# Kernel optimization log

Hardware: AMD Instinct MI355X
Metric: run time of the kernel (lower is better)

The kernel has to match this reference:

```python
import jax, jax.numpy as jnp
import numpy as np

DILATIONS = [1, 2, 4, 8, 12, 24]
NUM_ITER = 10
W1 = 0.3
EPS = 1e-8
# 8-neighborhood offsets of the one-hot 3x3 kernel (center excluded)
OFFSETS = [(0, 0), (0, 1), (0, 2), (1, 0), (1, 2), (2, 0), (2, 1), (2, 2)]


def resize_bilinear_ac(x, oh, ow):
    """Bilinear resize with align_corners=True on the last two dims."""
    H, W = x.shape[-2], x.shape[-1]
    ys = jnp.linspace(0.0, H - 1.0, oh)
    xs = jnp.linspace(0.0, W - 1.0, ow)
    y0 = jnp.floor(ys).astype(jnp.int32)
    y1 = jnp.minimum(y0 + 1, H - 1)
    wy = (ys - y0).astype(x.dtype)
    x0 = jnp.floor(xs).astype(jnp.int32)
    x1 = jnp.minimum(x0 + 1, W - 1)
    wx = (xs - x0).astype(x.dtype)
    r = x[..., y0, :] * (1.0 - wy)[:, None] + x[..., y1, :] * wy[:, None]
    return r[..., x0] * (1.0 - wx) + r[..., x1] * wx


def dilated_neighbors(x, dilations):
    """Replicate-pad + gather 8 dilated neighbors per dilation.
    x: [b,c,h,w] -> [b,c,8*len(dilations),h,w] (matches one-hot conv2d emulation)."""
    b, c, h, w = x.shape
    outs = []
    for d in dilations:
        xp = jnp.pad(x, ((0, 0), (0, 0), (d, d), (d, d)), mode='edge')
        for ki, kj in OFFSETS:
            outs.append(xp[:, :, d * ki:d * ki + h, d * kj:d * kj + w])
    return jnp.stack(outs, axis=2)


def make_pos(dilations):
    base = jnp.ones(8, dtype=jnp.float32)
    base = base.at[jnp.array([0, 2, 5, 7])].set(np.sqrt(2.0).astype(np.float32))
    return jnp.concatenate([base * d for d in dilations])  # [8*D]


def setup_inputs() -> dict:
    key = jax.random.key(0)
    k1, k2 = jax.random.split(key)
    imgs = jax.random.normal(k1, (1, 3, 224, 224), dtype=jnp.float32)
    masks = jax.random.uniform(k2, (1, 21, 56, 56), dtype=jnp.float32)
    return {"imgs": imgs, "masks": masks}


def reference(imgs, masks):
    b, c, h, w = imgs.shape
    # upsample masks to image resolution
    masks = resize_bilinear_ac(masks, h, w)
    # low-res branch (scale_factor=0.3, floor like torch)
    h2, w2 = int(h * 0.3), int(w * 0.3)
    imgs2 = resize_bilinear_ac(imgs, h2, w2)

    n2 = dilated_neighbors(imgs2, DILATIONS)                     # [1,3,K,h2,w2]
    abs2 = jnp.abs(n2 - imgs2[:, :, None])
    std2 = jnp.std(n2, axis=2, keepdims=True, ddof=1)
    aff2 = (-(abs2 / (std2 + EPS)) ** 2).mean(axis=1, keepdims=True)  # [1,1,K,h2,w2]

    n1 = dilated_neighbors(imgs, DILATIONS)                      # [1,3,K,h,w]
    abs1 = jnp.abs(n1 - imgs[:, :, None])
    std1 = jnp.std(n1, axis=2, keepdims=True, ddof=1)
    aff = (-(abs1 / (std1 + EPS) / W1) ** 2).mean(axis=1, keepdims=True)  # [1,1,K,h,w]

    pos = make_pos(DILATIONS)                                    # [K]
    pos_std = jnp.std(pos, ddof=1)
    pos_aff = -((pos / (pos_std + EPS) / W1) ** 2)               # [K]

    # squeeze(0) -> bilinear upsample -> unsqueeze(0)
    aff2_up = resize_bilinear_ac(aff2[0], h, w)[None]            # [1,1,K,h,w]

    aff_total = (jax.nn.softmax(aff, axis=2)
                 + jax.nn.softmax(aff2_up, axis=2)
                 + jax.nn.softmax(pos_aff)[None, None, :, None, None])

    for _ in range(NUM_ITER):
        nm = dilated_neighbors(masks, DILATIONS)                 # [1,21,K,h,w]
        masks = (nm * aff_total).sum(axis=2)
    return masks
```

## Files before the change

kernel.cpp:

```cpp
#include <hip/hip_runtime.h>
#include <hip/hip_fp16.h>
#include <math.h>

namespace {
constexpr int IH = 224, IW = 224;
constexpr int H2 = 67, W2 = 67;
constexpr int MH = 56, MW = 56;
constexpr int CI = 3, CM = 21;
constexpr int ND = 6;
constexpr int K = 48;
constexpr int HW = IH * IW;
constexpr int HW2 = H2 * W2;
constexpr float EPS = 1e-8f;
__device__ __constant__ int DILS_C[ND] = {1, 2, 4, 8, 12, 24};
}

struct PosArr { float v[K]; };

__device__ __forceinline__ float wsum64(float v) {
    #pragma unroll
    for (int off = 1; off < 64; off <<= 1) v += __shfl_xor(v, off);
    return v;
}

__global__ void k_img_down(const float* __restrict__ img, float* __restrict__ img2) {
    int t = blockIdx.x * blockDim.x + threadIdx.x;
    if (t >= CI * HW2) return;
    int c = t / HW2, r = t % HW2;
    int y = r / W2, x = r % W2;
    float fy = (float)y * ((float)(IH - 1) / (float)(H2 - 1));
    float fx = (float)x * ((float)(IW - 1) / (float)(W2 - 1));
    int y0 = (int)floorf(fy); int y1 = min(y0 + 1, IH - 1); float wy = fy - (float)y0;
    int x0 = (int)floorf(fx); int x1 = min(x0 + 1, IW - 1); float wx = fx - (float)x0;
    const float* p = img + c * HW;
    float v00 = p[y0 * IW + x0], v01 = p[y0 * IW + x1];
    float v10 = p[y1 * IW + x0], v11 = p[y1 * IW + x1];
    float r0 = v00 * (1.f - wy) + v10 * wy;
    float r1 = v01 * (1.f - wy) + v11 * wy;
    img2[t] = r0 * (1.f - wx) + r1 * wx;
}

__global__ void k_aff2(const float* __restrict__ img2, float* __restrict__ aff2) {
    int gtid = blockIdx.x * blockDim.x + threadIdx.x;
    int wave = gtid >> 6;
    int lane = threadIdx.x & 63;
    if (wave >= HW2) return;
    int t = wave;
    int y = t / W2, x = t % W2;

    int k = (lane < K) ? lane : (K - 1);
    int di = k >> 3, o = k & 7;
    int d = DILS_C[di];
    int ym = max(y - d, 0), yp = min(y + d, H2 - 1);
    int xm = max(x - d, 0), xp = min(x + d, W2 - 1);
    int ki = (0x22211000u >> (o * 4)) & 3;
    int kj = (0x21020210u >> (o * 4)) & 3;
    int ry = ki == 0 ? ym : (ki == 1 ? y : yp);
    int rx = kj == 0 ? xm : (kj == 1 ? x : xp);
    int nidx = ry * W2 + rx;

    float av = 0.f;
    #pragma unroll
    for (int c = 0; c < CI; ++c) {
        const float* p = img2 + c * HW2;
        float center = p[y * W2 + x];
        float v = p[nidx];
        float vv = (lane < K) ? v : 0.f;
        float s = wsum64(vv);
        float s2 = wsum64(vv * vv);
        float mean = s * (1.f / (float)K);
        float ss = s2 - (float)K * mean * mean;
        float stdv = sqrtf(fmaxf(ss, 0.f) * (1.f / (float)(K - 1)));
        float inv = 1.f / (stdv + EPS);
        float tt = fabsf(v - center) * inv;
        av += tt * tt;
    }
    if (lane < K) aff2[(size_t)t * K + k] = av;
}

__global__ void k_aff_total(const float* __restrict__ img,
                            const float* __restrict__ aff2,
                            __half* __restrict__ afft, PosArr pos) {
    int gid = blockIdx.x * blockDim.x + threadIdx.x;
    int t = gid >> 4;
    int lane = threadIdx.x & 15;
    if (t >= HW) return;
    int y = t / IW, x = t % IW;

    int nidx[3];
    int kk[3];
    #pragma unroll
    for (int s = 0; s < 3; ++s) {
        int k = lane + 16 * s;
        kk[s] = k;
        int di = k >> 3, o = k & 7;
        int d = DILS_C[di];
        int ki = (0x22211000u >> (o * 4)) & 3;
        int kj = (0x21020210u >> (o * 4)) & 3;
        int ym = max(y - d, 0), yp = min(y + d, IH - 1);
        int xm = max(x - d, 0), xp = min(x + d, IW - 1);
        int ry = ki == 0 ? ym : (ki == 1 ? y : yp);
        int rx = kj == 0 ? xm : (kj == 1 ? x : xp);
        nidx[s] = ry * IW + rx;
    }

    float av0 = 0.f, av1 = 0.f, av2 = 0.f;
    #pragma unroll
    for (int c = 0; c < CI; ++c) {
        const float* p = img + c * HW;
        float center = p[y * IW + x];
        float n0 = p[nidx[0]], n1 = p[nidx[1]], n2 = p[nidx[2]];
        float s1 = n0 + n1 + n2;
        float s2 = n0 * n0 + n1 * n1 + n2 * n2;
        #pragma unroll
        for (int off = 1; off < 16; off <<= 1) {
            s1 += __shfl_xor(s1, off, 16);
            s2 += __shfl_xor(s2, off, 16);
        }
        float mean = s1 * (1.f / (float)K);
        float ss = s2 - (float)K * mean * mean;
        float inv = 1.f / (sqrtf(fmaxf(ss, 0.f) * (1.f / (float)(K - 1))) + EPS);
        float t0 = fabsf(n0 - center) * inv; av0 += t0 * t0;
        float t1 = fabsf(n1 - center) * inv; av1 += t1 * t1;
        float t2 = fabsf(n2 - center) * inv; av2 += t2 * t2;
    }
    const float sc = -(1.f / (float)CI) / (0.3f * 0.3f);
    av0 *= sc; av1 *= sc; av2 *= sc;
    float m1 = fmaxf(av0, fmaxf(av1, av2));
    #pragma unroll
    for (int off = 1; off < 16; off <<= 1) m1 = fmaxf(m1, __shfl_xor(m1, off, 16));
    float e0 = expf(av0 - m1), e1 = expf(av1 - m1), e2 = expf(av2 - m1);
    float es = e0 + e1 + e2;
    #pragma unroll
    for (int off = 1; off < 16; off <<= 1) es += __shfl_xor(es, off, 16);
    float r1 = 1.f / es;

    float fy = (float)y * ((float)(H2 - 1) / (float)(IH - 1));
    float fx = (float)x * ((float)(W2 - 1) / (float)(IW - 1));
    int y0 = (int)floorf(fy); int y1 = min(y0 + 1, H2 - 1); float wy = fy - (float)y0;
    int x0 = (int)floorf(fx); int x1 = min(x0 + 1, W2 - 1); float wx = fx - (float)x0;
    const float* q00 = aff2 + (size_t)(y0 * W2 + x0) * K;
    const float* q01 = aff2 + (size_t)(y0 * W2 + x1) * K;
    const float* q10 = aff2 + (size_t)(y1 * W2 + x0) * K;
    const float* q11 = aff2 + (size_t)(y1 * W2 + x1) * K;
    float w00 = (1.f - wy) * (1.f - wx), w01 = (1.f - wy) * wx;
    float w10 = wy * (1.f - wx), w11 = wy * wx;
    const float sc2 = -(1.f / (float)CI);
    float b0 = (q00[kk[0]] * w00 + q01[kk[0]] * w01 + q10[kk[0]] * w10 + q11[kk[0]] * w11) * sc2;
    float b1 = (q00[kk[1]] * w00 + q01[kk[1]] * w01 + q10[kk[1]] * w10 + q11[kk[1]] * w11) * sc2;
    float b2 = (q00[kk[2]] * w00 + q01[kk[2]] * w01 + q10[kk[2]] * w10 + q11[kk[2]] * w11) * sc2;
    float m2 = fmaxf(b0, fmaxf(b1, b2));
    #pragma unroll
    for (int off = 1; off < 16; off <<= 1) m2 = fmaxf(m2, __shfl_xor(m2, off, 16));
    float f0 = expf(b0 - m2), f1 = expf(b1 - m2), f2 = expf(b2 - m2);
    float fs = f0 + f1 + f2;
    #pragma unroll
    for (int off = 1; off < 16; off <<= 1) fs += __shfl_xor(fs, off, 16);
    float r2 = 1.f / fs;

    __half* o = afft + (size_t)t * K;
    o[kk[0]] = __float2half(e0 * r1 + f0 * r2 + pos.v[kk[0]]);
    o[kk[1]] = __float2half(e1 * r1 + f1 * r2 + pos.v[kk[1]]);
    o[kk[2]] = __float2half(e2 * r1 + f2 * r2 + pos.v[kk[2]]);
}

__global__ void k_mask_up(const float* __restrict__ m, float* __restrict__ mu) {
    int t = blockIdx.x * blockDim.x + threadIdx.x;
    if (t >= CM * HW) return;
    int c = t / HW, r = t % HW;
    int y = r / IW, x = r % IW;
    float fy = (float)y * ((float)(MH - 1) / (float)(IH - 1));
    float fx = (float)x * ((float)(MW - 1) / (float)(IW - 1));
    int y0 = (int)floorf(fy); int y1 = min(y0 + 1, MH - 1); float wy = fy - (float)y0;
    int x0 = (int)floorf(fx); int x1 = min(x0 + 1, MW - 1); float wx = fx - (float)x0;
    const float* p = m + c * MH * MW;
    float v00 = p[y0 * MW + x0], v01 = p[y0 * MW + x1];
    float v10 = p[y1 * MW + x0], v11 = p[y1 * MW + x1];
    float r0 = v00 * (1.f - wy) + v10 * wy;
    float r1 = v01 * (1.f - wy) + v11 * wy;
    mu[t] = r0 * (1.f - wx) + r1 * wx;
}

__global__ __launch_bounds__(256) void k_prop(const float* __restrict__ min_,
                                              const __half* __restrict__ afft,
                                              float* __restrict__ mout) {
    __shared__ float L[13 * 224];
    int tid = threadIdx.x;
    int bid = blockIdx.x;
    int sw = (bid & 7) * 588 + (bid >> 3);
    int y = sw / 21;
    int c = sw - y * 21;

    int x = min(tid, IW - 1);
    int t = y * IW + x;
    uint4 w[6];
    {
        const uint4* aw = (const uint4*)(afft + (size_t)t * K);
        #pragma unroll
        for (int i = 0; i < 6; ++i) w[i] = aw[i];
    }

    const int ROW_DY[13] = {-24, -12, -8, -4, -2, -1, 0, 1, 2, 4, 8, 12, 24};
    const float* mc = min_ + (size_t)c * HW;
    for (int i = tid; i < 13 * 56; i += 256) {
        int r = i / 56;
        int xq = i - r * 56;
        int gy = min(max(y + ROW_DY[r], 0), IH - 1);
        *(float4*)(L + r * 224 + xq * 4) = ((const float4*)(mc + gy * IW))[xq];
    }
    __syncthreads();

    if (tid >= IW) return;

    const int DILS[ND] = {1, 2, 4, 8, 12, 24};
    const int RMI[ND] = {5, 4, 3, 2, 1, 0};
    const int RPI[ND] = {7, 8, 9, 10, 11, 12};
    const float* Lc = L + 6 * 224;

    float acc = 0.f;
    #pragma unroll
    for (int di = 0; di < ND; ++di) {
        int d = DILS[di];
        int cm = max(x - d, 0);
        int cp = min(x + d, IW - 1);
        const float* Lm = L + RMI[di] * 224;
        const float* Lp = L + RPI[di] * 224;
        const __half2* hp = (const __half2*)&w[di];
        float2 f01 = __half22float2(hp[0]);
        float2 f23 = __half22float2(hp[1]);
        float2 f45 = __half22float2(hp[2]);
        float2 f67 = __half22float2(hp[3]);
        acc += Lm[cm] * f01.x;
        acc += Lm[x]  * f01.y;
        acc += Lm[cp] * f23.x;
        acc += Lc[cm] * f23.y;
        acc += Lc[cp] * f45.x;
        acc += Lp[cm] * f45.y;
        acc += Lp[x]  * f67.x;
        acc += Lp[cp] * f67.y;
    }
    mout[(size_t)c * HW + t] = acc;
}

extern "C" void kernel_launch(void* const* d_in, const int* in_sizes, int n_in,
                              void* d_out, int out_size, void* d_ws, size_t ws_size,
                              hipStream_t stream) {
    const float* imgs  = (const float*)d_in[0];
    const float* masks = (const float*)d_in[1];
    float* out = (float*)d_out;

    float* ws = (float*)d_ws;
    float* imgs2 = ws;
    float* aff2  = imgs2 + 16384;
    __half* afft = (__half*)(aff2 + K * HW2);
    float* mA    = aff2 + K * HW2 + (K * HW) / 2;
    float* mB    = mA + (size_t)CM * HW;

    PosArr pos;
    {
        double pv[K];
        const int dil[ND] = {1, 2, 4, 8, 12, 24};
        const double s2 = sqrt(2.0);
        for (int di = 0; di < ND; ++di)
            for (int o = 0; o < 8; ++o) {
                double base = (o == 0 || o == 2 || o == 5 || o == 7) ? s2 : 1.0;
                pv[di * 8 + o] = base * (double)dil[di];
            }
        double sum = 0.0; for (int k = 0; k < K; ++k) sum += pv[k];
        double mean = sum / K;
        double ssd = 0.0; for (int k = 0; k < K; ++k) { double d0 = pv[k] - mean; ssd += d0 * d0; }
        double stdv = sqrt(ssd / (K - 1));
        double pa[K];
        double mx = -1e300;
        for (int k = 0; k < K; ++k) {
            double u = pv[k] / (stdv + 1e-8) / 0.3;
            pa[k] = -u * u;
            if (pa[k] > mx) mx = pa[k];
        }
        double es = 0.0, ev[K];
        for (int k = 0; k < K; ++k) { ev[k] = exp(pa[k] - mx); es += ev[k]; }
        for (int k = 0; k < K; ++k) pos.v[k] = (float)(ev[k] / es);
    }

    dim3 blk(256);
    k_img_down<<<(CI * HW2 + 255) / 256, blk, 0, stream>>>(imgs, imgs2);
    k_aff2<<<(HW2 * 64 + 255) / 256, blk, 0, stream>>>(imgs2, aff2);
    k_aff_total<<<(HW * 16 + 255) / 256, blk, 0, stream>>>(imgs, aff2, afft, pos);
    k_mask_up<<<(CM * HW + 255) / 256, blk, 0, stream>>>(masks, mA);

    float* bufs[2] = {mA, mB};
    const float* cur = mA;
    for (int i = 0; i < 10; ++i) {
        float* o = (i == 9) ? out : bufs[(i + 1) & 1];
        k_prop<<<4704, dim3(256), 0, stream>>>(cur, afft, o);
        cur = o;
    }
}
```

Baseline: 205.4 us.

## Process three row-channel tiles per block with register-prefetched next tile

Each propagation block now handles three (row, channel) work items instead of one. While computing the current item, it prefetches the next item's 13 mask rows into registers, then stores them to shared memory between two barriers. The grid shrinks threefold and launch bounds request higher occupancy. This aims to hide global load latency behind compute and amortise block launch cost. In exchange it adds register pressure and extra barriers, and leaves fewer blocks to spread across the GPU.

```diff
diff --git a/kernel.cpp b/kernel.cpp
--- a/kernel.cpp
+++ b/kernel.cpp
@@ -181,65 +181,109 @@
     mu[t] = r0 * (1.f - wx) + r1 * wx;
 }
 
-__global__ __launch_bounds__(256) void k_prop(const float* __restrict__ min_,
-                                              const __half* __restrict__ afft,
-                                              float* __restrict__ mout) {
+__global__ __launch_bounds__(256, 8) void k_prop(const float* __restrict__ min_,
+                                                 const __half* __restrict__ afft,
+                                                 float* __restrict__ mout) {
     __shared__ float L[13 * 224];
-    int tid = threadIdx.x;
-    int bid = blockIdx.x;
-    int sw = (bid & 7) * 588 + (bid >> 3);
-    int y = sw / 21;
-    int c = sw - y * 21;
-
-    int x = min(tid, IW - 1);
-    int t = y * IW + x;
-    uint4 w[6];
+    const int tid = threadIdx.x;
+    const int b = blockIdx.x;
+    const int base = (b & 7) * 588 + (b >> 3);
+    const int ROW_DY[13] = {-24, -12, -8, -4, -2, -1, 0, 1, 2, 4, 8, 12, 24};
+
     {
-        const uint4* aw = (const uint4*)(afft + (size_t)t * K);
-        #pragma unroll
-        for (int i = 0; i < 6; ++i) w[i] = aw[i];
-    }
-
-    const int ROW_DY[13] = {-24, -12, -8, -4, -2, -1, 0, 1, 2, 4, 8, 12, 24};
-    const float* mc = min_ + (size_t)c * HW;
-    for (int i = tid; i < 13 * 56; i += 256) {
-        int r = i / 56;
-        int xq = i - r * 56;
-        int gy = min(max(y + ROW_DY[r], 0), IH - 1);
-        *(float4*)(L + r * 224 + xq * 4) = ((const float4*)(mc + gy * IW))[xq];
+        int sw = base;
+        int y = sw / 21, c = sw - y * 21;
+        const float* mc = min_ + (size_t)c * HW;
+        for (int i = tid; i < 13 * 56; i += 256) {
+            int r = i / 56, q = i - r * 56;
+            int gy = min(max(y + ROW_DY[r], 0), IH - 1);
+            *(float4*)(L + r * 224 + q * 4) = ((const float4*)(mc + gy * IW))[q];
+        }
     }
     __syncthreads();
 
-    if (tid >= IW) return;
-
-    const int DILS[ND] = {1, 2, 4, 8, 12, 24};
-    const int RMI[ND] = {5, 4, 3, 2, 1, 0};
-    const int RPI[ND] = {7, 8, 9, 10, 11, 12};
-    const float* Lc = L + 6 * 224;
-
-    float acc = 0.f;
-    #pragma unroll
-    for (int di = 0; di < ND; ++di) {
-        int d = DILS[di];
-        int cm = max(x - d, 0);
-        int cp = min(x + d, IW - 1);
-        const float* Lm = L + RMI[di] * 224;
-        const float* Lp = L + RPI[di] * 224;
-        const __half2* hp = (const __half2*)&w[di];
-        float2 f01 = __half22float2(hp[0]);
-        float2 f23 = __half22float2(hp[1]);
-        float2 f45 = __half22float2(hp[2]);
-        float2 f67 = __half22float2(hp[3]);
-        acc += Lm[cm] * f01.x;
-        acc += Lm[x]  * f01.y;
-        acc += Lm[cp] * f23.x;
-        acc += Lc[cm] * f23.y;
-        acc += Lc[cp] * f45.x;
-        acc += Lp[cm] * f45.y;
-        acc += Lp[x]  * f67.x;
-        acc += Lp[cp] * f67.y;
-    }
-    mout[(size_t)c * HW + t] = acc;
+    #pragma unroll
+    for (int j = 0; j < 3; ++j) {
+        const int sw = base + j * 196;
+        const int y = sw / 21, c = sw - y * 21;
+
+        float4 s0, s1, s2;
+        if (j < 2) {
+            int sw2 = base + (j + 1) * 196;
+            int y2 = sw2 / 21, c2 = sw2 - y2 * 21;
+            const float* mc2 = min_ + (size_t)c2 * HW;
+            {
+                int i = tid; int r = i / 56, q = i - r * 56;
+                int gy = min(max(y2 + ROW_DY[r], 0), IH - 1);
+                s0 = ((const float4*)(mc2 + gy * IW))[q];
+            }
+            {
+                int i = tid + 256; int r = i / 56, q = i - r * 56;
+                int gy = min(max(y2 + ROW_DY[r], 0), IH - 1);
+                s1 = ((const float4*)(mc2 + gy * IW))[q];
+            }
+            if (tid < 216) {
+                int i = tid + 512; int r = i / 56, q = i - r * 56;
+                int gy = min(max(y2 + ROW_DY[r], 0), IH - 1);
+                s2 = ((const float4*)(mc2 + gy * IW))[q];
+            }
+        }
+
+        if (tid < IW) {
+            const int x = tid;
+            const int t = y * IW + x;
+            uint4 w[6];
+            {
+                const uint4* aw = (const uint4*)(afft + (size_t)t * K);
+                #pragma unroll
+                for (int i = 0; i < 6; ++i) w[i] = aw[i];
+            }
+            const int DILS[ND] = {1, 2, 4, 8, 12, 24};
+            const int RMI[ND] = {5, 4, 3, 2, 1, 0};
+            const int RPI[ND] = {7, 8, 9, 10, 11, 12};
+            const float* Lc = L + 6 * 224;
+            float acc = 0.f;
+            #pragma unroll
+            for (int di = 0; di < ND; ++di) {
+                int d = DILS[di];
+                int cm = max(x - d, 0);
+                int cp = min(x + d, IW - 1);
+                const float* Lm = L + RMI[di] * 224;
+                const float* Lp = L + RPI[di] * 224;
+                const __half2* hp = (const __half2*)&w[di];
+                float2 f01 = __half22float2(hp[0]);
+                float2 f23 = __half22float2(hp[1]);
+                float2 f45 = __half22float2(hp[2]);
+                float2 f67 = __half22float2(hp[3]);
+                acc += Lm[cm] * f01.x;
+                acc += Lm[x]  * f01.y;
+                acc += Lm[cp] * f23.x;
+                acc += Lc[cm] * f23.y;
+                acc += Lc[cp] * f45.x;
+                acc += Lp[cm] * f45.y;
+                acc += Lp[x]  * f67.x;
+                acc += Lp[cp] * f67.y;
+            }
+            mout[(size_t)c * HW + t] = acc;
+        }
+
+        if (j < 2) {
+            __syncthreads();
+            {
+                int i = tid; int r = i / 56, q = i - r * 56;
+                *(float4*)(L + r * 224 + q * 4) = s0;
+            }
+            {
+                int i = tid + 256; int r = i / 56, q = i - r * 56;
+                *(float4*)(L + r * 224 + q * 4) = s1;
+            }
+            if (tid < 216) {
+                int i = tid + 512; int r = i / 56, q = i - r * 56;
+                *(float4*)(L + r * 224 + q * 4) = s2;
+            }
+            __syncthreads();
+        }
+    }
 }
 
 extern "C" void kernel_launch(void* const* d_in, const int* in_sizes, int n_in,
@@ -292,7 +336,7 @@
     const float* cur = mA;
     for (int i = 0; i < 10; ++i) {
         float* o = (i == 9) ? out : bufs[(i + 1) & 1];
-        k_prop<<<4704, dim3(256), 0, stream>>>(cur, afft, o);
+        k_prop<<<1568, blk, 0, stream>>>(cur, afft, o);
         cur = o;
     }
 }
```

Result: slower. 237.7 us (+15.7%).
